# Kernel optimization log

Hardware: AMD Instinct MI355X
Metric: run time of the kernel (lower is better)

The kernel has to match this reference:

```python
import jax, jax.numpy as jnp
import numpy as np

B, GS, IN, HID = 256, 32, 512, 1024
HW = GS * GS

def setup_inputs() -> dict:
    key = jax.random.key(0)
    ks = jax.random.split(key, 18)
    s = 0.02
    return {
        "grid": jax.random.normal(ks[0], (B, 1, GS, GS), jnp.float32),
        "conv1_w": jax.random.normal(ks[1], (8, 1, 3, 3), jnp.float32) * s,
        "conv1_b": jax.random.normal(ks[2], (8,), jnp.float32) * s,
        "conv2_w": jax.random.normal(ks[3], (16, 8, 3, 3), jnp.float32) * s,
        "conv2_b": jax.random.normal(ks[4], (16,), jnp.float32) * s,
        "lin_w": jax.random.normal(ks[5], (IN, HW * 16), jnp.float32) * s,
        "lin_b": jax.random.normal(ks[6], (IN,), jnp.float32) * s,
        "gru_wih": jax.random.normal(ks[7], (3 * HID, IN + HW + 1), jnp.float32) * s,
        "gru_whh": jax.random.normal(ks[8], (3 * HID, HID), jnp.float32) * s,
        "gru_bih": jax.random.normal(ks[9], (3 * HID,), jnp.float32) * s,
        "gru_bhh": jax.random.normal(ks[10], (3 * HID,), jnp.float32) * s,
        "write_w": jax.random.normal(ks[11], (HW, HID), jnp.float32) * s,
        "write_b": jax.random.normal(ks[12], (HW,), jnp.float32) * s,
        "inc_w": jax.random.normal(ks[13], (1, HID), jnp.float32) * s,
        "inc_b": jax.random.normal(ks[14], (1,), jnp.float32) * s,
        "term_w": jax.random.normal(ks[15], (1, HID), jnp.float32) * s,
        "term_b": jax.random.normal(ks[16], (1,), jnp.float32) * s,
        "max_steps": 100,
    }

def _conv(x, w, b):
    y = jax.lax.conv_general_dilated(x, w, (1, 1), "SAME",
                                     dimension_numbers=("NCHW", "OIHW", "NCHW"))
    return y + b[None, :, None, None]

def _gru_cell(x, h, wih, whh, bih, bhh):
    gi = x @ wih.T + bih            # (B, 3H)
    gh = h @ whh.T + bhh
    ir, iz, inn = jnp.split(gi, 3, axis=1)
    hr, hz, hn = jnp.split(gh, 3, axis=1)
    r = jax.nn.sigmoid(ir + hr)
    z = jax.nn.sigmoid(iz + hz)
    n = jnp.tanh(inn + r * hn)
    return (1.0 - z) * n + z * h

def reference(grid, conv1_w, conv1_b, conv2_w, conv2_b, lin_w, lin_b,
              gru_wih, gru_whh, gru_bih, gru_bhh,
              write_w, write_b, inc_w, inc_b, term_w, term_b, max_steps):
    bsz = grid.shape[0]
    feat = jax.nn.relu(_conv(grid, conv1_w, conv1_b))
    feat = jax.nn.relu(_conv(feat, conv2_w, conv2_b))
    feat = feat.reshape(bsz, -1) @ lin_w.T + lin_b     # (B, IN), torch Flatten is channel-major

    def step(carry, _):
        h, mask, count, done = carry
        x = jnp.concatenate([feat, mask, count], axis=1)
        h2 = _gru_cell(x, h, gru_wih, gru_whh, gru_bih, gru_bhh)
        write = jax.nn.sigmoid(h2 @ write_w.T + write_b)
        inc = jax.nn.sigmoid(h2 @ inc_w.T + inc_b)
        term = jax.nn.sigmoid(h2 @ term_w.T + term_b)
        upd = jnp.logical_not(done)
        h_n = jnp.where(upd, h2, h)
        mask_n = jnp.where(upd, mask + write, mask)
        count_n = jnp.where(upd, count + inc, count)
        done_n = jnp.logical_or(done, jnp.all(term > 0.5))
        return (h_n, mask_n, count_n, done_n), None

    init = (jnp.zeros((bsz, HID), grid.dtype),
            jnp.zeros((bsz, HW), grid.dtype),
            jnp.zeros((bsz, 1), grid.dtype),
            jnp.array(False))
    (h, mask, count, done), _ = jax.lax.scan(step, init, None, length=max_steps)
    return count, mask
```

## Files before the change

kernel.cpp:

```cpp
#include <hip/hip_runtime.h>
#include <hip/hip_cooperative_groups.h>

namespace cg = cooperative_groups;

#define DEVI static __device__ __forceinline__

typedef __attribute__((ext_vector_type(8))) short s8v;
typedef __attribute__((ext_vector_type(4))) float f32x4;
typedef unsigned short us_t;
typedef unsigned int u32;

constexpr int NT_ = 256;
constexpr int B_ = 256, HW_ = 1024, IN_ = 512, HID_ = 1024, H3_ = 3072;
constexpr int XD_ = 1537;
constexpr int FLAT_ = 16384;

constexpr int OFF_WIHFBF = 0;
constexpr int OFF_WIHM2  = 393216;
constexpr int OFF_WHHBF  = 3538944;
constexpr int OFF_WIHC   = 5111808;
constexpr int OFF_CNTD   = 5114880;
constexpr int OFF_FLAGS  = 5115136;
constexpr int OFF_FEATBF = 5115264;
constexpr int OFF_GI     = 5180800;
constexpr int OFF_GH     = 5967232;
constexpr int OFF_H0     = 6753664;
constexpr int OFF_H1     = 7015808;
constexpr int OFF_WSIG   = 7277952;
constexpr int OFF_HHI    = 7540096;
constexpr int OFF_WSIG2  = 7671168;
constexpr int OFF_C2BF   = 7933312;
constexpr int OFF_LINWBF = 10030464;
constexpr int OFF_PART = OFF_GI;
constexpr int OFF_PA   = OFF_C2BF;
constexpr int OFF_WWBF = 10292608;

struct Params {
  const float* grid;
  const float* c1w; const float* c1b;
  const float* c2w; const float* c2b;
  const float* linw; const float* linb;
  const float* wih; const float* whh;
  const float* bih; const float* bhh;
  const float* ww;  const float* wb;
  const float* incw; const float* incb;
  const float* termw; const float* termb;
  const int* max_steps;
  float* out;
  float* ws;
};

DEVI float sigm(float x) { return 1.f / (1.f + __expf(-x)); }
DEVI float tanh_(float x) { return 1.f - 2.f / (__expf(2.f * x) + 1.f); }
DEVI float2 ld2(const float* p) { return *(const float2*)p; }
DEVI void ld4(float* d, const float* p) {
  float4 v = *(const float4*)p; d[0] = v.x; d[1] = v.y; d[2] = v.z; d[3] = v.w;
}
DEVI us_t f2bf(float x) {
  union { float f; u32 u; } v; v.f = x;
  u32 r = v.u + 0x7FFFu + ((v.u >> 16) & 1u);
  return (us_t)(r >> 16);
}
DEVI float bf2f(us_t h) {
  union { u32 u; float f; } v; v.u = ((u32)h) << 16; return v.f;
}
DEVI u32 pack2(float a, float b) { return (u32)f2bf(a) | ((u32)f2bf(b) << 16); }

__global__ __launch_bounds__(NT_) void conv_kernel(Params p) {
  __shared__ float s_in[34 * 34];
  __shared__ float s_c1[8 * 34 * 34];
  const int b = blockIdx.x;
  const int tid = threadIdx.x;
  for (int i = tid; i < 34 * 34; i += NT_) s_in[i] = 0.f;
  for (int i = tid; i < 8 * 34 * 34; i += NT_) s_c1[i] = 0.f;
  __syncthreads();
  for (int i = tid; i < 1024; i += NT_) {
    int y = i >> 5, x = i & 31;
    s_in[(y + 1) * 34 + (x + 1)] = p.grid[b * 1024 + i];
  }
  __syncthreads();
  const int pos0 = tid * 4;
  const int y = pos0 >> 5, x0 = pos0 & 31;
  {
    float win[3][6];
    #pragma unroll
    for (int dy = 0; dy < 3; ++dy)
      #pragma unroll
      for (int c = 0; c < 6; ++c) win[dy][c] = s_in[(y + dy) * 34 + x0 + c];
    float acc[8][4];
    #pragma unroll
    for (int oc = 0; oc < 8; ++oc)
      #pragma unroll
      for (int i = 0; i < 4; ++i) acc[oc][i] = p.c1b[oc];
    #pragma unroll
    for (int oc = 0; oc < 8; ++oc)
      #pragma unroll
      for (int dy = 0; dy < 3; ++dy)
        #pragma unroll
        for (int dx = 0; dx < 3; ++dx) {
          float w = p.c1w[oc * 9 + dy * 3 + dx];
          #pragma unroll
          for (int i = 0; i < 4; ++i)
            acc[oc][i] = fmaf(w, win[dy][i + dx], acc[oc][i]);
        }
    #pragma unroll
    for (int oc = 0; oc < 8; ++oc)
      #pragma unroll
      for (int i = 0; i < 4; ++i)
        s_c1[oc * 1156 + (y + 1) * 34 + (x0 + i + 1)] = fmaxf(acc[oc][i], 0.f);
  }
  __syncthreads();
  {
    float acc[16][4];
    #pragma unroll
    for (int oc = 0; oc < 16; ++oc)
      #pragma unroll
      for (int i = 0; i < 4; ++i) acc[oc][i] = p.c2b[oc];
    for (int ic = 0; ic < 8; ++ic) {
      float win[3][6];
      #pragma unroll
      for (int dy = 0; dy < 3; ++dy)
        #pragma unroll
        for (int c = 0; c < 6; ++c)
          win[dy][c] = s_c1[ic * 1156 + (y + dy) * 34 + x0 + c];
      #pragma unroll
      for (int oc = 0; oc < 16; ++oc)
        #pragma unroll
        for (int dy = 0; dy < 3; ++dy)
          #pragma unroll
          for (int dx = 0; dx < 3; ++dx) {
            float w = p.c2w[oc * 72 + ic * 9 + dy * 3 + dx];
            #pragma unroll
            for (int i = 0; i < 4; ++i)
              acc[oc][i] = fmaf(w, win[dy][i + dx], acc[oc][i]);
          }
    }
    us_t* dst = (us_t*)(p.ws + OFF_C2BF) + b * FLAT_;
    #pragma unroll
    for (int oc = 0; oc < 16; ++oc) {
      u32 lo = pack2(fmaxf(acc[oc][0], 0.f), fmaxf(acc[oc][1], 0.f));
      u32 hi = pack2(fmaxf(acc[oc][2], 0.f), fmaxf(acc[oc][3], 0.f));
      *(uint2*)(dst + oc * 1024 + pos0) = make_uint2(lo, hi);
    }
  }
}

__global__ __launch_bounds__(NT_) void prep_kernel(Params p) {
  const int gt = blockIdx.x * NT_ + threadIdx.x;
  const int gs = gridDim.x * NT_;
  us_t* wihf = (us_t*)(p.ws + OFF_WIHFBF);
  us_t* wihm2 = (us_t*)(p.ws + OFF_WIHM2);
  us_t* whhbf = (us_t*)(p.ws + OFF_WHHBF);
  us_t* linwbf = (us_t*)(p.ws + OFF_LINWBF);
  float* wihc = p.ws + OFF_WIHC;
  int* flags = (int*)(p.ws + OFF_FLAGS);
  for (int i = gt; i < (IN_ * FLAT_) / 4; i += gs) {
    float4 v = *(const float4*)(p.linw + (size_t)i * 4);
    *(uint2*)(linwbf + (size_t)i * 4) = make_uint2(pack2(v.x, v.y), pack2(v.z, v.w));
  }
  for (int i = gt; i < (H3_ * HID_) / 4; i += gs) {
    float4 v = *(const float4*)(p.whh + (size_t)i * 4);
    *(uint2*)(whhbf + (size_t)i * 4) = make_uint2(pack2(v.x, v.y), pack2(v.z, v.w));
  }
  for (int i = gt; i < H3_ * IN_; i += gs) {
    int n = i >> 9, k = i & 511;
    wihf[i] = f2bf(p.wih[n * XD_ + k]);
  }
  for (int i = gt; i < H3_ * HID_; i += gs) {
    int n = i >> 10, k = i & 1023;
    float v = p.wih[n * XD_ + 512 + k];
    us_t hi = f2bf(v);
    wihm2[n * 2048 + k] = hi;
    wihm2[n * 2048 + 1024 + k] = f2bf(v - bf2f(hi));
  }
  for (int i = gt; i < H3_; i += gs) wihc[i] = p.wih[i * XD_ + 1536];
  for (int i = gt; i < 128; i += gs) flags[i] = 1;
}

DEVI void mfma_block(const us_t* __restrict__ Ag, int lda,
                     const us_t* __restrict__ Bg, int ldb, int nc,
                     us_t* __restrict__ sA, us_t* __restrict__ sB,
                     float* __restrict__ dst, int ldd) {
  const int tid = threadIdx.x;
  const int ar = tid >> 3, au = tid & 7;
  const int sw = au ^ (ar & 7);
  const int abase = (ar * 8 + sw) * 8;
  const us_t* a0p = Ag + (size_t)ar * lda + au * 8;
  const us_t* a1p = Ag + (size_t)(ar + 32) * lda + au * 8;
  const us_t* b0p = Bg + (size_t)ar * ldb + au * 8;
  const us_t* b1p = b0p + (size_t)32 * ldb;
  const us_t* b2p = b0p + (size_t)64 * ldb;
  const us_t* b3p = b0p + (size_t)96 * ldb;
  f32x4 acc[4][2];
  #pragma unroll
  for (int f = 0; f < 4; ++f) { acc[f][0] = (f32x4)0.f; acc[f][1] = (f32x4)0.f; }
  s8v ra0 = *(const s8v*)a0p;
  s8v ra1 = *(const s8v*)a1p;
  s8v rb0 = *(const s8v*)b0p;
  s8v rb1 = *(const s8v*)b1p;
  s8v rb2 = *(const s8v*)b2p;
  s8v rb3 = *(const s8v*)b3p;
  const int w = tid >> 6;
  const int lane = tid & 63;
  const int l15 = lane & 15, l4 = lane >> 4;
  const int rsw = l15 & 7;
  int c = 0;
  for (;;) {
    __syncthreads();
    *(s8v*)(sA + abase) = ra0;
    *(s8v*)(sA + abase + 2048) = ra1;
    *(s8v*)(sB + abase) = rb0;
    *(s8v*)(sB + abase + 2048) = rb1;
    *(s8v*)(sB + abase + 4096) = rb2;
    *(s8v*)(sB + abase + 6144) = rb3;
    ++c;
    if (c < nc) {
      const int ko = c * 64;
      ra0 = *(const s8v*)(a0p + ko);
      ra1 = *(const s8v*)(a1p + ko);
      rb0 = *(const s8v*)(b0p + ko);
      rb1 = *(const s8v*)(b1p + ko);
      rb2 = *(const s8v*)(b2p + ko);
      rb3 = *(const s8v*)(b3p + ko);
    }
    __syncthreads();
    #pragma unroll
    for (int kk = 0; kk < 2; ++kk) {
      const int uoff = ((kk * 4 + l4) ^ rsw) * 8;
      s8v bA = *(const s8v*)(sB + (w * 32 + l15) * 64 + uoff);
      s8v bB = *(const s8v*)(sB + (w * 32 + 16 + l15) * 64 + uoff);
      #pragma unroll
      for (int f = 0; f < 4; ++f) {
        s8v a = *(const s8v*)(sA + (f * 16 + l15) * 64 + uoff);
        acc[f][0] = __builtin_amdgcn_mfma_f32_16x16x32_bf16(a, bA, acc[f][0], 0, 0, 0);
        acc[f][1] = __builtin_amdgcn_mfma_f32_16x16x32_bf16(a, bB, acc[f][1], 0, 0, 0);
      }
    }
    if (c >= nc) break;
  }
  #pragma unroll
  for (int f = 0; f < 4; ++f)
    #pragma unroll
    for (int g = 0; g < 2; ++g) {
      float* dp = dst + (size_t)(f * 16 + l4 * 4) * ldd + w * 32 + g * 16 + l15;
      #pragma unroll
      for (int j = 0; j < 4; ++j) dp[(size_t)j * ldd] = acc[f][g][j];
    }
}

__global__ __launch_bounds__(NT_) void lin_mfma(Params p) {
  __shared__ us_t sm[12288];
  const int b = blockIdx.x;
  const int ks = b & 15, t = b >> 4;
  const int mt = t >> 2, nt = t & 3;
  const us_t* A = (us_t*)(p.ws + OFF_C2BF) + (size_t)mt * 64 * FLAT_ + ks * 1024;
  const us_t* B = (us_t*)(p.ws + OFF_LINWBF) + (size_t)nt * 128 * FLAT_ + ks * 1024;
  float* dst = p.ws + OFF_PART + ks * (B_ * IN_) + mt * 64 * IN_ + nt * 128;
  mfma_block(A, FLAT_, B, FLAT_, 16, sm, sm + 4096, dst, IN_);
}

__global__ __launch_bounds__(NT_) void red_kernel(Params p) {
  const int gt = blockIdx.x * NT_ + threadIdx.x;
  {
    const int o = gt & (IN_ - 1);
    const float* part = p.ws + OFF_PART;
    float s = p.linb[o];
    #pragma unroll
    for (int ks = 0; ks < 16; ++ks) s += part[ks * (B_ * IN_) + gt];
    ((us_t*)(p.ws + OFF_FEATBF))[gt] = f2bf(s);
  }
  us_t* wwbf = (us_t*)(p.ws + OFF_WWBF);
  #pragma unroll
  for (int r = 0; r < 2; ++r) {
    const int j = gt + r * 131072;
    float4 v = *(const float4*)(p.ww + (size_t)j * 4);
    *(uint2*)(wwbf + (size_t)j * 4) = make_uint2(pack2(v.x, v.y), pack2(v.z, v.w));
  }
}

__global__ __launch_bounds__(NT_) void a1_mfma(Params p) {
  __shared__ us_t sm[12288];
  const int b = blockIdx.x;
  const int mt = b / 24, nt = b - mt * 24;
  const us_t* A = (us_t*)(p.ws + OFF_FEATBF) + (size_t)mt * 64 * IN_;
  const us_t* B = (us_t*)(p.ws + OFF_WIHFBF) + (size_t)nt * 128 * IN_;
  float* dst = p.ws + OFF_GI + (size_t)mt * 64 * H3_ + nt * 128;
  mfma_block(A, IN_, B, IN_, 8, sm, sm + 4096, dst, H3_);
}

__global__ __launch_bounds__(NT_) void stepA_mfma(Params p, int step) {
  if (((volatile int*)(p.ws + OFF_FLAGS))[step - 1]) return;
  __shared__ us_t sm[12288];
  const int b = blockIdx.x;
  if (b < 288) {
    const int term = b / 96, r = b - term * 96;
    const int mt = r / 24, nt = r - mt * 24;
    const us_t* A = (us_t*)(p.ws + OFF_WSIG2) + (size_t)mt * 64 * 2048 +
                    (term == 1 ? 1024 : 0);
    const us_t* B = (us_t*)(p.ws + OFF_WIHM2) + (size_t)nt * 128 * 2048 +
                    (term == 2 ? 1024 : 0);
    float* dst = p.ws + OFF_PA + (size_t)term * (B_ * H3_) + (size_t)mt * 64 * H3_ + nt * 128;
    mfma_block(A, 2048, B, 2048, 16, sm, sm + 4096, dst, H3_);
  } else {
    const int r = b - 288;
    const int mt = r / 24, nt = r - mt * 24;
    const us_t* A = (us_t*)(p.ws + OFF_HHI) + (size_t)mt * 64 * HID_;
    const us_t* B = (us_t*)(p.ws + OFF_WHHBF) + (size_t)nt * 128 * HID_;
    float* dst = p.ws + OFF_GH + (size_t)mt * 64 * H3_ + nt * 128;
    mfma_block(A, HID_, B, HID_, 16, sm, sm + 4096, dst, H3_);
  }
}

__global__ __launch_bounds__(NT_) void stepG_kernel(Params p, int step) {
  int* flags = (int*)(p.ws + OFF_FLAGS);
  if (step > 0 && ((volatile int*)flags)[step - 1]) return;
  __shared__ float sred[8];
  const int row = blockIdx.x;
  const int tid = threadIdx.x;
  const size_t base = (size_t)row * H3_;
  float* const gi = p.ws + OFF_GI + base;
  const float* const gh = p.ws + OFF_GH + base;
  const float* const pA = p.ws + OFF_PA;
  const float* const wihc = p.ws + OFF_WIHC;
  const float* hold = p.ws + ((step & 1) ? OFF_H1 : OFF_H0) + (size_t)row * HID_;
  float* hnew = p.ws + ((step & 1) ? OFF_H0 : OFF_H1) + (size_t)row * HID_;
  us_t* hhi = (us_t*)(p.ws + OFF_HHI) + (size_t)row * HID_;
  const float cd = (step > 0) ? (p.ws + OFF_CNTD)[row] : 0.f;
  float incd = 0.f, termd = 0.f;
  #pragma unroll
  for (int q = 0; q < 4; ++q) {
    const int c = tid + q * NT_;
    float gr_ = gi[c], gz_ = gi[1024 + c], gn_ = gi[2048 + c];
    float hr_ = 0.f, hz_ = 0.f, hn_ = 0.f, hv = 0.f;
    if (step > 0) {
      gr_ += pA[base + c] + pA[786432 + base + c] + pA[1572864 + base + c] +
             cd * wihc[c];
      gz_ += pA[base + 1024 + c] + pA[786432 + base + 1024 + c] +
             pA[1572864 + base + 1024 + c] + cd * wihc[1024 + c];
      gn_ += pA[base + 2048 + c] + pA[786432 + base + 2048 + c] +
             pA[1572864 + base + 2048 + c] + cd * wihc[2048 + c];
      gi[c] = gr_; gi[1024 + c] = gz_; gi[2048 + c] = gn_;
      hr_ = gh[c]; hz_ = gh[1024 + c]; hn_ = gh[2048 + c];
      hv = hold[c];
    }
    float rr = sigm(gr_ + p.bih[c] + hr_ + p.bhh[c]);
    float zz = sigm(gz_ + p.bih[1024 + c] + hz_ + p.bhh[1024 + c]);
    float nn = tanh_(gn_ + p.bih[2048 + c] + rr * (hn_ + p.bhh[2048 + c]));
    float h2 = (1.f - zz) * nn + zz * hv;
    hnew[c] = h2;
    hhi[c] = f2bf(h2);
    incd = fmaf(h2, p.incw[c], incd);
    termd = fmaf(h2, p.termw[c], termd);
  }
  #pragma unroll
  for (int off = 32; off > 0; off >>= 1) {
    incd += __shfl_down(incd, off);
    termd += __shfl_down(termd, off);
  }
  if ((tid & 63) == 0) { sred[tid >> 6] = incd; sred[4 + (tid >> 6)] = termd; }
  __syncthreads();
  if (tid == 0) {
    float it = sred[0] + sred[1] + sred[2] + sred[3];
    float tt = sred[4] + sred[5] + sred[6] + sred[7];
    float cdn = sigm(it + p.incb[0]);
    (p.ws + OFF_CNTD)[row] = cdn;
    p.out[row] += cdn;
    if (tt + p.termb[0] <= 0.f) atomicAnd(&flags[step], 0);
  }
}

__global__ __launch_bounds__(NT_) void stepW_mfma(Params p, int step) {
  if (step > 0 && ((volatile int*)(p.ws + OFF_FLAGS))[step - 1]) return;
  __shared__ us_t sm[12288];
  const int b = blockIdx.x;
  const int ks = b & 7, t = b >> 3;
  const int mt = t >> 3, nt = t & 7;
  const us_t* A = (us_t*)(p.ws + OFF_HHI) + (size_t)mt * 64 * HID_ + ks * 128;
  const us_t* B = (us_t*)(p.ws + OFF_WWBF) + (size_t)nt * 128 * HID_ + ks * 128;
  float* dst = p.ws + OFF_PA + ks * (B_ * HW_) + (size_t)mt * 64 * HW_ + nt * 128;
  mfma_block(A, HID_, B, HID_, 2, sm, sm + 4096, dst, HW_);
}

__global__ __launch_bounds__(NT_) void stepWepi_kernel(Params p, int step) {
  if (step > 0 && ((volatile int*)(p.ws + OFF_FLAGS))[step - 1]) return;
  const int i = (blockIdx.x * NT_ + threadIdx.x) * 4;
  const int m = i >> 10, n = i & 1023;
  const float* pW = p.ws + OFF_PA;
  float4 s = *(const float4*)(p.wb + n);
  #pragma unroll
  for (int ks = 0; ks < 8; ++ks) {
    float4 v = *(const float4*)(pW + ks * (B_ * HW_) + i);
    s.x += v.x; s.y += v.y; s.z += v.z; s.w += v.w;
  }
  float4 sv = {sigm(s.x), sigm(s.y), sigm(s.z), sigm(s.w)};
  float* op = p.out + B_ + i;
  float4 ov = *(float4*)op;
  ov.x += sv.x; ov.y += sv.y; ov.z += sv.z; ov.w += sv.w;
  *(float4*)op = ov;
  *(float4*)(p.ws + OFF_WSIG + i) = sv;
  us_t* w2 = (us_t*)(p.ws + OFF_WSIG2) + (size_t)m * 2048 + n;
  us_t h0 = f2bf(sv.x), h1 = f2bf(sv.y), h2b = f2bf(sv.z), h3 = f2bf(sv.w);
  *(uint2*)w2 = make_uint2((u32)h0 | ((u32)h1 << 16), (u32)h2b | ((u32)h3 << 16));
  *(uint2*)(w2 + 1024) = make_uint2(
      pack2(sv.x - bf2f(h0), sv.y - bf2f(h1)),
      pack2(sv.z - bf2f(h2b), sv.w - bf2f(h3)));
}

DEVI void b_job(const Params& p, float* sh2, float* swb,
                const float* gi, const float* gh, const float* hold,
                float* hnew, float* wsig, float* cntd, int* dflag, int job) {
  const int tid = threadIdx.x;
  const int mt = job >> 3, nt = job & 7;
  const int r0 = mt * 8, c0 = nt * 128;
  const int gr = tid >> 5;
  const int gk = (tid & 31) * 2;
  const int wr = tid & 7;
  const int wc = (tid >> 3) * 4;
  const int row = r0 + gr;
  const float* giR = gi + row * H3_;
  const float* ghR = gh + row * H3_;
  const float* hR = hold + row * HID_;
  float* hW = hnew + row * HID_;
  float acc[4] = {0.f, 0.f, 0.f, 0.f};
  float incd = 0.f, termd = 0.f;
  const bool wh = (nt == 0);
  for (int kc = 0; kc < HID_; kc += 64) {
    float2 gxr = ld2(giR + kc + gk);
    float2 gxz = ld2(giR + 1024 + kc + gk);
    float2 gxn = ld2(giR + 2048 + kc + gk);
    float2 ghr = ld2(ghR + kc + gk);
    float2 ghz = ld2(ghR + 1024 + kc + gk);
    float2 ghn = ld2(ghR + 2048 + kc + gk);
    float2 hol = ld2(hR + kc + gk);
    float2 bri = ld2(p.bih + kc + gk);
    float2 brh = ld2(p.bhh + kc + gk);
    float2 bzi = ld2(p.bih + 1024 + kc + gk);
    float2 bzh = ld2(p.bhh + 1024 + kc + gk);
    float2 bni = ld2(p.bih + 2048 + kc + gk);
    float2 bnh = ld2(p.bhh + 2048 + kc + gk);
    float2 iw = ld2(p.incw + kc + gk);
    float2 tw = ld2(p.termw + kc + gk);
    float h2[2];
    {
      float rr = sigm(gxr.x + bri.x + ghr.x + brh.x);
      float zz = sigm(gxz.x + bzi.x + ghz.x + bzh.x);
      float nn = tanh_(gxn.x + bni.x + rr * (ghn.x + bnh.x));
      h2[0] = (1.f - zz) * nn + zz * hol.x;
      rr = sigm(gxr.y + bri.y + ghr.y + brh.y);
      zz = sigm(gxz.y + bzi.y + ghz.y + bzh.y);
      nn = tanh_(gxn.y + bni.y + rr * (ghn.y + bnh.y));
      h2[1] = (1.f - zz) * nn + zz * hol.y;
    }
    incd = fmaf(h2[0], iw.x, fmaf(h2[1], iw.y, incd));
    termd = fmaf(h2[0], tw.x, fmaf(h2[1], tw.y, termd));
    float4 wreg[8];
    #pragma unroll
    for (int it = 0; it < 8; ++it) {
      int id = tid + it * 256;
      int c = id >> 4, k4 = (id & 15) * 4;
      wreg[it] = *(const float4*)(p.ww + (c0 + c) * HID_ + kc + k4);
    }
    __syncthreads();
    sh2[gr * 68 + gk] = h2[0];
    sh2[gr * 68 + gk + 1] = h2[1];
    #pragma unroll
    for (int it = 0; it < 8; ++it) {
      int id = tid + it * 256;
      int c = id >> 4, k4 = (id & 15) * 4;
      swb[(k4 + 0) * 132 + c] = wreg[it].x;
      swb[(k4 + 1) * 132 + c] = wreg[it].y;
      swb[(k4 + 2) * 132 + c] = wreg[it].z;
      swb[(k4 + 3) * 132 + c] = wreg[it].w;
    }
    if (wh) {
      *(float2*)(hW + kc + gk) = make_float2(h2[0], h2[1]);
      *(u32*)((us_t*)(p.ws + OFF_HHI) + row * HID_ + kc + gk) = pack2(h2[0], h2[1]);
    }
    __syncthreads();
    #pragma unroll 8
    for (int kk = 0; kk < 64; ++kk) {
      float a = sh2[wr * 68 + kk];
      float4 b = *(const float4*)(swb + kk * 132 + wc);
      acc[0] = fmaf(a, b.x, acc[0]);
      acc[1] = fmaf(a, b.y, acc[1]);
      acc[2] = fmaf(a, b.z, acc[2]);
      acc[3] = fmaf(a, b.w, acc[3]);
    }
  }
  if (wh) {
    #pragma unroll
    for (int off = 16; off > 0; off >>= 1) {
      incd += __shfl_down(incd, off, 32);
      termd += __shfl_down(termd, off, 32);
    }
    if ((tid & 31) == 0) {
      float cd = sigm(incd + p.incb[0]);
      cntd[row] = cd;
      p.out[row] += cd;
      if (termd + p.termb[0] <= 0.f) atomicAnd(dflag, 0);
    }
  }
  {
    const int m = r0 + wr;
    float4 wb4 = *(const float4*)(p.wb + c0 + wc);
    float4 sv = {sigm(acc[0] + wb4.x), sigm(acc[1] + wb4.y),
                 sigm(acc[2] + wb4.z), sigm(acc[3] + wb4.w)};
    float* op = p.out + B_ + m * HW_ + c0 + wc;
    float4 ov = *(float4*)op;
    ov.x += sv.x; ov.y += sv.y; ov.z += sv.z; ov.w += sv.w;
    *(float4*)op = ov;
    *(float4*)(wsig + m * HID_ + c0 + wc) = sv;
    us_t* w2 = (us_t*)(p.ws + OFF_WSIG2) + m * 2048 + c0 + wc;
    us_t h0 = f2bf(sv.x), h1 = f2bf(sv.y), h2b = f2bf(sv.z), h3 = f2bf(sv.w);
    *(uint2*)w2 = make_uint2((u32)h0 | ((u32)h1 << 16), (u32)h2b | ((u32)h3 << 16));
    *(uint2*)(w2 + 1024) = make_uint2(
        pack2(sv.x - bf2f(h0), sv.y - bf2f(h1)),
        pack2(sv.z - bf2f(h2b), sv.w - bf2f(h3)));
  }
}

template <bool SB>
DEVI void gemm_db64(const float* __restrict__ A, int lda,
                    const float* __restrict__ Bw, int ldb, int K,
                    float* __restrict__ As, float* __restrict__ Bs,
                    float (&acc)[4][4]) {
  constexpr int P = 68;
  const int tid = threadIdx.x;
  const int tx = tid & 15, ty = tid >> 4;
  const int lr = tid >> 2, lk = (tid & 3) << 2;
  #pragma unroll
  for (int i = 0; i < 4; ++i)
    #pragma unroll
    for (int j = 0; j < 4; ++j) acc[i][j] = 0.f;
  auto ldb4 = [&](int k0) {
    float4 v;
    if constexpr (SB) {
      const float* q = Bw + (size_t)lr * ldb + k0 + lk;
      v.x = q[0]; v.y = q[1]; v.z = q[2]; v.w = q[3];
    } else {
      v = *(const float4*)(Bw + (size_t)lr * ldb + k0 + lk);
    }
    return v;
  };
  float4 va = *(const float4*)(A + lr * lda + lk);
  float4 vb = ldb4(0);
  As[(lk + 0) * P + lr] = va.x; As[(lk + 1) * P + lr] = va.y;
  As[(lk + 2) * P + lr] = va.z; As[(lk + 3) * P + lr] = va.w;
  Bs[(lk + 0) * P + lr] = vb.x; Bs[(lk + 1) * P + lr] = vb.y;
  Bs[(lk + 2) * P + lr] = vb.z; Bs[(lk + 3) * P + lr] = vb.w;
  __syncthreads();
  int cur = 0;
  for (int k0 = 16; k0 < K; k0 += 16) {
    va = *(const float4*)(A + lr * lda + k0 + lk);
    vb = ldb4(k0);
    const float* as = As + cur * (16 * P);
    const float* bs = Bs + cur * (16 * P);
    #pragma unroll
    for (int kk = 0; kk < 16; ++kk) {
      float a[4], b[4];
      ld4(a, as + kk * P + ty * 4);
      ld4(b, bs + kk * P + tx * 4);
      #pragma unroll
      for (int i = 0; i < 4; ++i)
        #pragma unroll
        for (int j = 0; j < 4; ++j) acc[i][j] = fmaf(a[i], b[j], acc[i][j]);
    }
    __syncthreads();
    float* asw = As + (cur ^ 1) * (16 * P);
    float* bsw = Bs + (cur ^ 1) * (16 * P);
    asw[(lk + 0) * P + lr] = va.x; asw[(lk + 1) * P + lr] = va.y;
    asw[(lk + 2) * P + lr] = va.z; asw[(lk + 3) * P + lr] = va.w;
    bsw[(lk + 0) * P + lr] = vb.x; bsw[(lk + 1) * P + lr] = vb.y;
    bsw[(lk + 2) * P + lr] = vb.z; bsw[(lk + 3) * P + lr] = vb.w;
    __syncthreads();
    cur ^= 1;
  }
  const float* as = As + cur * (16 * P);
  const float* bs = Bs + cur * (16 * P);
  #pragma unroll
  for (int kk = 0; kk < 16; ++kk) {
    float a[4], b[4];
    ld4(a, as + kk * P + ty * 4);
    ld4(b, bs + kk * P + tx * 4);
    #pragma unroll
    for (int i = 0; i < 4; ++i)
      #pragma unroll
      for (int j = 0; j < 4; ++j) acc[i][j] = fmaf(a[i], b[j], acc[i][j]);
  }
}

__global__ __launch_bounds__(NT_, 2) void tail_kernel(Params p, int start) {
  int* flags = (int*)(p.ws + OFF_FLAGS);
  if (((volatile int*)flags)[start - 1]) return;
  cg::grid_group gg = cg::this_grid();
  __shared__ __align__(16) float smem[8992];
  float* As = smem;
  float* Bs = smem + 2176;
  float* sh2 = smem;
  float* swb = smem + 544;
  float* const ws = p.ws;
  float* const gi = ws + OFF_GI;
  float* const gh = ws + OFF_GH;
  float* const wsig = ws + OFF_WSIG;
  float* const cntd = ws + OFF_CNTD;
  const float* const wihc = ws + OFF_WIHC;
  const int tid = threadIdx.x;
  const int bid = blockIdx.x;
  const int nb = gridDim.x;
  const int tx = tid & 15, ty = tid >> 4;
  const int msteps = p.max_steps[0];

  for (int step = start; step < msteps; ++step) {
    float* hcur = ws + ((step & 1) ? OFF_H1 : OFF_H0);
    float* hnxt = ws + ((step & 1) ? OFF_H0 : OFF_H1);
    for (int job = bid; job < 384; job += nb) {
      float acc[4][4];
      if (job < 192) {
        const int mt = job / 48, nt = job - mt * 48;
        gemm_db64<true>(wsig + mt * 64 * HID_, HID_,
                        p.wih + (size_t)nt * 64 * XD_ + 512, XD_, HID_, As, Bs, acc);
        #pragma unroll
        for (int i = 0; i < 4; ++i) {
          const int m = mt * 64 + ty * 4 + i;
          const float cd = cntd[m];
          float4 wc4 = *(const float4*)(wihc + nt * 64 + tx * 4);
          float* gp = gi + m * H3_ + nt * 64 + tx * 4;
          float4 g = *(float4*)gp;
          g.x += acc[i][0] + cd * wc4.x;
          g.y += acc[i][1] + cd * wc4.y;
          g.z += acc[i][2] + cd * wc4.z;
          g.w += acc[i][3] + cd * wc4.w;
          *(float4*)gp = g;
        }
      } else {
        const int j = job - 192;
        const int mt = j / 48, nt = j - mt * 48;
        gemm_db64<false>(hcur + mt * 64 * HID_, HID_,
                         p.whh + (size_t)nt * 64 * HID_, HID_, HID_, As, Bs, acc);
        #pragma unroll
        for (int i = 0; i < 4; ++i) {
          float4 v = {acc[i][0], acc[i][1], acc[i][2], acc[i][3]};
          *(float4*)(gh + (mt * 64 + ty * 4 + i) * H3_ + nt * 64 + tx * 4) = v;
        }
      }
      __syncthreads();
    }
    gg.sync();
    for (int job = bid; job < 256; job += nb)
      b_job(p, sh2, swb, gi, gh, hcur, hnxt, wsig, cntd, &flags[step], job);
    gg.sync();
    if (((volatile int*)flags)[step]) break;
  }
}

extern "C" void kernel_launch(void* const* d_in, const int* in_sizes, int n_in,
                              void* d_out, int out_size, void* d_ws, size_t ws_size,
                              hipStream_t stream) {
  (void)in_sizes; (void)n_in; (void)ws_size;
  Params prm;
  prm.grid = (const float*)d_in[0];
  prm.c1w  = (const float*)d_in[1];
  prm.c1b  = (const float*)d_in[2];
  prm.c2w  = (const float*)d_in[3];
  prm.c2b  = (const float*)d_in[4];
  prm.linw = (const float*)d_in[5];
  prm.linb = (const float*)d_in[6];
  prm.wih  = (const float*)d_in[7];
  prm.whh  = (const float*)d_in[8];
  prm.bih  = (const float*)d_in[9];
  prm.bhh  = (const float*)d_in[10];
  prm.ww   = (const float*)d_in[11];
  prm.wb   = (const float*)d_in[12];
  prm.incw = (const float*)d_in[13];
  prm.incb = (const float*)d_in[14];
  prm.termw = (const float*)d_in[15];
  prm.termb = (const float*)d_in[16];
  prm.max_steps = (const int*)d_in[17];
  prm.out = (float*)d_out;
  prm.ws = (float*)d_ws;

  hipLaunchKernelGGL(conv_kernel, dim3(B_), dim3(NT_), 0, stream, prm);
  hipLaunchKernelGGL(prep_kernel, dim3(2048), dim3(NT_), 0, stream, prm);
  hipLaunchKernelGGL(lin_mfma, dim3(256), dim3(NT_), 0, stream, prm);
  hipLaunchKernelGGL(red_kernel, dim3(512), dim3(NT_), 0, stream, prm);
  hipMemsetAsync(d_out, 0, (size_t)out_size * sizeof(float), stream);
  hipLaunchKernelGGL(a1_mfma, dim3(96), dim3(NT_), 0, stream, prm);

  constexpr int U = 3;
  hipLaunchKernelGGL(stepG_kernel, dim3(B_), dim3(NT_), 0, stream, prm, 0);
  hipLaunchKernelGGL(stepW_mfma, dim3(256), dim3(NT_), 0, stream, prm, 0);
  hipLaunchKernelGGL(stepWepi_kernel, dim3(256), dim3(NT_), 0, stream, prm, 0);
  for (int t = 1; t < U; ++t) {
    hipLaunchKernelGGL(stepA_mfma, dim3(384), dim3(NT_), 0, stream, prm, t);
    hipLaunchKernelGGL(stepG_kernel, dim3(B_), dim3(NT_), 0, stream, prm, t);
    hipLaunchKernelGGL(stepW_mfma, dim3(256), dim3(NT_), 0, stream, prm, t);
    hipLaunchKernelGGL(stepWepi_kernel, dim3(256), dim3(NT_), 0, stream, prm, t);
  }
  int start = U;
  void* args[] = {(void*)&prm, (void*)&start};
  (void)hipLaunchCooperativeKernel((const void*)tail_kernel, dim3(384), dim3(NT_),
                                   args, 0, stream);
}
```

Before: 155.5 us.

## Fuse conv and prep kernels, split-K stepA GEMMs, drop output memset

Merges the conv and weight-prep kernels into one launch with block-index dispatch, and splits the stepA GEMMs along K into two halves (768 blocks instead of 384), writing eight partial buffers that stepG sums. The output memset is removed; step 0 now writes the outputs directly instead of accumulating. The number of unrolled multi-kernel steps before the cooperative tail kernel drops from 3 to 2. Together these aim to cut launch overhead and raise GPU occupancy for the per-step GEMMs, at the cost of extra partial-sum traffic and a larger workspace.

```diff
diff --git a/kernel.cpp b/kernel.cpp
--- a/kernel.cpp
+++ b/kernel.cpp
@@ -32,8 +32,9 @@
 constexpr int OFF_C2BF   = 7933312;
 constexpr int OFF_LINWBF = 10030464;
 constexpr int OFF_PART = OFF_GI;
-constexpr int OFF_PA   = OFF_C2BF;
+constexpr int OFF_PW   = OFF_C2BF;
 constexpr int OFF_WWBF = 10292608;
+constexpr int OFF_PA2  = 14224768;
 
 struct Params {
   const float* grid;
@@ -66,115 +67,116 @@
 }
 DEVI u32 pack2(float a, float b) { return (u32)f2bf(a) | ((u32)f2bf(b) << 16); }
 
-__global__ __launch_bounds__(NT_) void conv_kernel(Params p) {
-  __shared__ float s_in[34 * 34];
-  __shared__ float s_c1[8 * 34 * 34];
-  const int b = blockIdx.x;
+__global__ __launch_bounds__(NT_) void front_kernel(Params p) {
+  __shared__ float smem[34 * 34 + 8 * 34 * 34];
   const int tid = threadIdx.x;
-  for (int i = tid; i < 34 * 34; i += NT_) s_in[i] = 0.f;
-  for (int i = tid; i < 8 * 34 * 34; i += NT_) s_c1[i] = 0.f;
-  __syncthreads();
-  for (int i = tid; i < 1024; i += NT_) {
-    int y = i >> 5, x = i & 31;
-    s_in[(y + 1) * 34 + (x + 1)] = p.grid[b * 1024 + i];
-  }
-  __syncthreads();
-  const int pos0 = tid * 4;
-  const int y = pos0 >> 5, x0 = pos0 & 31;
-  {
-    float win[3][6];
-    #pragma unroll
-    for (int dy = 0; dy < 3; ++dy)
-      #pragma unroll
-      for (int c = 0; c < 6; ++c) win[dy][c] = s_in[(y + dy) * 34 + x0 + c];
-    float acc[8][4];
-    #pragma unroll
-    for (int oc = 0; oc < 8; ++oc)
-      #pragma unroll
-      for (int i = 0; i < 4; ++i) acc[oc][i] = p.c1b[oc];
-    #pragma unroll
-    for (int oc = 0; oc < 8; ++oc)
+  if (blockIdx.x < 256) {
+    float* s_in = smem;
+    float* s_c1 = smem + 34 * 34;
+    const int b = blockIdx.x;
+    for (int i = tid; i < 34 * 34; i += NT_) s_in[i] = 0.f;
+    for (int i = tid; i < 8 * 34 * 34; i += NT_) s_c1[i] = 0.f;
+    __syncthreads();
+    for (int i = tid; i < 1024; i += NT_) {
+      int y = i >> 5, x = i & 31;
+      s_in[(y + 1) * 34 + (x + 1)] = p.grid[b * 1024 + i];
+    }
+    __syncthreads();
+    const int pos0 = tid * 4;
+    const int y = pos0 >> 5, x0 = pos0 & 31;
+    {
+      float win[3][6];
       #pragma unroll
       for (int dy = 0; dy < 3; ++dy)
         #pragma unroll
-        for (int dx = 0; dx < 3; ++dx) {
-          float w = p.c1w[oc * 9 + dy * 3 + dx];
-          #pragma unroll
-          for (int i = 0; i < 4; ++i)
-            acc[oc][i] = fmaf(w, win[dy][i + dx], acc[oc][i]);
-        }
-    #pragma unroll
-    for (int oc = 0; oc < 8; ++oc)
-      #pragma unroll
-      for (int i = 0; i < 4; ++i)
-        s_c1[oc * 1156 + (y + 1) * 34 + (x0 + i + 1)] = fmaxf(acc[oc][i], 0.f);
-  }
-  __syncthreads();
-  {
-    float acc[16][4];
-    #pragma unroll
-    for (int oc = 0; oc < 16; ++oc)
-      #pragma unroll
-      for (int i = 0; i < 4; ++i) acc[oc][i] = p.c2b[oc];
-    for (int ic = 0; ic < 8; ++ic) {
-      float win[3][6];
-      #pragma unroll
-      for (int dy = 0; dy < 3; ++dy)
-        #pragma unroll
-        for (int c = 0; c < 6; ++c)
-          win[dy][c] = s_c1[ic * 1156 + (y + dy) * 34 + x0 + c];
-      #pragma unroll
-      for (int oc = 0; oc < 16; ++oc)
+        for (int c = 0; c < 6; ++c) win[dy][c] = s_in[(y + dy) * 34 + x0 + c];
+      float acc[8][4];
+      #pragma unroll
+      for (int oc = 0; oc < 8; ++oc)
+        #pragma unroll
+        for (int i = 0; i < 4; ++i) acc[oc][i] = p.c1b[oc];
+      #pragma unroll
+      for (int oc = 0; oc < 8; ++oc)
         #pragma unroll
         for (int dy = 0; dy < 3; ++dy)
           #pragma unroll
           for (int dx = 0; dx < 3; ++dx) {
-            float w = p.c2w[oc * 72 + ic * 9 + dy * 3 + dx];
+            float w = p.c1w[oc * 9 + dy * 3 + dx];
             #pragma unroll
             for (int i = 0; i < 4; ++i)
               acc[oc][i] = fmaf(w, win[dy][i + dx], acc[oc][i]);
           }
-    }
-    us_t* dst = (us_t*)(p.ws + OFF_C2BF) + b * FLAT_;
-    #pragma unroll
-    for (int oc = 0; oc < 16; ++oc) {
-      u32 lo = pack2(fmaxf(acc[oc][0], 0.f), fmaxf(acc[oc][1], 0.f));
-      u32 hi = pack2(fmaxf(acc[oc][2], 0.f), fmaxf(acc[oc][3], 0.f));
-      *(uint2*)(dst + oc * 1024 + pos0) = make_uint2(lo, hi);
-    }
-  }
-}
-
-__global__ __launch_bounds__(NT_) void prep_kernel(Params p) {
-  const int gt = blockIdx.x * NT_ + threadIdx.x;
-  const int gs = gridDim.x * NT_;
-  us_t* wihf = (us_t*)(p.ws + OFF_WIHFBF);
-  us_t* wihm2 = (us_t*)(p.ws + OFF_WIHM2);
-  us_t* whhbf = (us_t*)(p.ws + OFF_WHHBF);
-  us_t* linwbf = (us_t*)(p.ws + OFF_LINWBF);
-  float* wihc = p.ws + OFF_WIHC;
-  int* flags = (int*)(p.ws + OFF_FLAGS);
-  for (int i = gt; i < (IN_ * FLAT_) / 4; i += gs) {
-    float4 v = *(const float4*)(p.linw + (size_t)i * 4);
-    *(uint2*)(linwbf + (size_t)i * 4) = make_uint2(pack2(v.x, v.y), pack2(v.z, v.w));
-  }
-  for (int i = gt; i < (H3_ * HID_) / 4; i += gs) {
-    float4 v = *(const float4*)(p.whh + (size_t)i * 4);
-    *(uint2*)(whhbf + (size_t)i * 4) = make_uint2(pack2(v.x, v.y), pack2(v.z, v.w));
-  }
-  for (int i = gt; i < H3_ * IN_; i += gs) {
-    int n = i >> 9, k = i & 511;
-    wihf[i] = f2bf(p.wih[n * XD_ + k]);
-  }
-  for (int i = gt; i < H3_ * HID_; i += gs) {
-    int n = i >> 10, k = i & 1023;
-    float v = p.wih[n * XD_ + 512 + k];
-    us_t hi = f2bf(v);
-    wihm2[n * 2048 + k] = hi;
-    wihm2[n * 2048 + 1024 + k] = f2bf(v - bf2f(hi));
-  }
-  for (int i = gt; i < H3_; i += gs) wihc[i] = p.wih[i * XD_ + 1536];
-  for (int i = gt; i < 128; i += gs) flags[i] = 1;
+      #pragma unroll
+      for (int oc = 0; oc < 8; ++oc)
+        #pragma unroll
+        for (int i = 0; i < 4; ++i)
+          s_c1[oc * 1156 + (y + 1) * 34 + (x0 + i + 1)] = fmaxf(acc[oc][i], 0.f);
+    }
+    __syncthreads();
+    {
+      float acc[16][4];
+      #pragma unroll
+      for (int oc = 0; oc < 16; ++oc)
+        #pragma unroll
+        for (int i = 0; i < 4; ++i) acc[oc][i] = p.c2b[oc];
+      for (int ic = 0; ic < 8; ++ic) {
+        float win[3][6];
+        #pragma unroll
+        for (int dy = 0; dy < 3; ++dy)
+          #pragma unroll
+          for (int c = 0; c < 6; ++c)
+            win[dy][c] = s_c1[ic * 1156 + (y + dy) * 34 + x0 + c];
+        #pragma unroll
+        for (int oc = 0; oc < 16; ++oc)
+          #pragma unroll
+          for (int dy = 0; dy < 3; ++dy)
+            #pragma unroll
+            for (int dx = 0; dx < 3; ++dx) {
+              float w = p.c2w[oc * 72 + ic * 9 + dy * 3 + dx];
+              #pragma unroll
+              for (int i = 0; i < 4; ++i)
+                acc[oc][i] = fmaf(w, win[dy][i + dx], acc[oc][i]);
+            }
+      }
+      us_t* dst = (us_t*)(p.ws + OFF_C2BF) + b * FLAT_;
+      #pragma unroll
+      for (int oc = 0; oc < 16; ++oc) {
+        u32 lo = pack2(fmaxf(acc[oc][0], 0.f), fmaxf(acc[oc][1], 0.f));
+        u32 hi = pack2(fmaxf(acc[oc][2], 0.f), fmaxf(acc[oc][3], 0.f));
+        *(uint2*)(dst + oc * 1024 + pos0) = make_uint2(lo, hi);
+      }
+    }
+  } else {
+    const int gt = (blockIdx.x - 256) * NT_ + tid;
+    const int gs = 2048 * NT_;
+    us_t* wihf = (us_t*)(p.ws + OFF_WIHFBF);
+    us_t* wihm2 = (us_t*)(p.ws + OFF_WIHM2);
+    us_t* whhbf = (us_t*)(p.ws + OFF_WHHBF);
+    us_t* linwbf = (us_t*)(p.ws + OFF_LINWBF);
+    float* wihc = p.ws + OFF_WIHC;
+    int* flags = (int*)(p.ws + OFF_FLAGS);
+    for (int i = gt; i < (IN_ * FLAT_) / 4; i += gs) {
+      float4 v = *(const float4*)(p.linw + (size_t)i * 4);
+      *(uint2*)(linwbf + (size_t)i * 4) = make_uint2(pack2(v.x, v.y), pack2(v.z, v.w));
+    }
+    for (int i = gt; i < (H3_ * HID_) / 4; i += gs) {
+      float4 v = *(const float4*)(p.whh + (size_t)i * 4);
+      *(uint2*)(whhbf + (size_t)i * 4) = make_uint2(pack2(v.x, v.y), pack2(v.z, v.w));
+    }
+    for (int i = gt; i < H3_ * IN_; i += gs) {
+      int n = i >> 9, k = i & 511;
+      wihf[i] = f2bf(p.wih[n * XD_ + k]);
+    }
+    for (int i = gt; i < H3_ * HID_; i += gs) {
+      int n = i >> 10, k = i & 1023;
+      float v = p.wih[n * XD_ + 512 + k];
+      us_t hi = f2bf(v);
+      wihm2[n * 2048 + k] = hi;
+      wihm2[n * 2048 + 1024 + k] = f2bf(v - bf2f(hi));
+    }
+    for (int i = gt; i < H3_; i += gs) wihc[i] = p.wih[i * XD_ + 1536];
+    for (int i = gt; i < 128; i += gs) flags[i] = 1;
+  }
 }
 
 DEVI void mfma_block(const us_t* __restrict__ Ag, int lda,
@@ -292,22 +294,29 @@
   if (((volatile int*)(p.ws + OFF_FLAGS))[step - 1]) return;
   __shared__ us_t sm[12288];
   const int b = blockIdx.x;
-  if (b < 288) {
-    const int term = b / 96, r = b - term * 96;
-    const int mt = r / 24, nt = r - mt * 24;
+  if (b < 576) {
+    const int term = b / 192;
+    const int r = b - term * 192;
+    const int ks = r / 96;
+    const int t = r - ks * 96;
+    const int mt = t / 24, nt = t - mt * 24;
     const us_t* A = (us_t*)(p.ws + OFF_WSIG2) + (size_t)mt * 64 * 2048 +
-                    (term == 1 ? 1024 : 0);
+                    (term == 1 ? 1024 : 0) + ks * 512;
     const us_t* B = (us_t*)(p.ws + OFF_WIHM2) + (size_t)nt * 128 * 2048 +
-                    (term == 2 ? 1024 : 0);
-    float* dst = p.ws + OFF_PA + (size_t)term * (B_ * H3_) + (size_t)mt * 64 * H3_ + nt * 128;
-    mfma_block(A, 2048, B, 2048, 16, sm, sm + 4096, dst, H3_);
+                    (term == 2 ? 1024 : 0) + ks * 512;
+    float* dst = p.ws + OFF_PA2 + (size_t)(term * 2 + ks) * 786432 +
+                 (size_t)mt * 64 * H3_ + nt * 128;
+    mfma_block(A, 2048, B, 2048, 8, sm, sm + 4096, dst, H3_);
   } else {
-    const int r = b - 288;
-    const int mt = r / 24, nt = r - mt * 24;
-    const us_t* A = (us_t*)(p.ws + OFF_HHI) + (size_t)mt * 64 * HID_;
-    const us_t* B = (us_t*)(p.ws + OFF_WHHBF) + (size_t)nt * 128 * HID_;
-    float* dst = p.ws + OFF_GH + (size_t)mt * 64 * H3_ + nt * 128;
-    mfma_block(A, HID_, B, HID_, 16, sm, sm + 4096, dst, H3_);
+    const int r = b - 576;
+    const int ks = r / 96;
+    const int t = r - ks * 96;
+    const int mt = t / 24, nt = t - mt * 24;
+    const us_t* A = (us_t*)(p.ws + OFF_HHI) + (size_t)mt * 64 * HID_ + ks * 512;
+    const us_t* B = (us_t*)(p.ws + OFF_WHHBF) + (size_t)nt * 128 * HID_ + ks * 512;
+    float* dst = p.ws + OFF_PA2 + (size_t)(6 + ks) * 786432 +
+                 (size_t)mt * 64 * H3_ + nt * 128;
+    mfma_block(A, HID_, B, HID_, 8, sm, sm + 4096, dst, H3_);
   }
 }
 
@@ -319,8 +328,7 @@
   const int tid = threadIdx.x;
   const size_t base = (size_t)row * H3_;
   float* const gi = p.ws + OFF_GI + base;
-  const float* const gh = p.ws + OFF_GH + base;
-  const float* const pA = p.ws + OFF_PA;
+  const float* const pA = p.ws + OFF_PA2;
   const float* const wihc = p.ws + OFF_WIHC;
   const float* hold = p.ws + ((step & 1) ? OFF_H1 : OFF_H0) + (size_t)row * HID_;
   float* hnew = p.ws + ((step & 1) ? OFF_H0 : OFF_H1) + (size_t)row * HID_;
@@ -333,14 +341,20 @@
     float gr_ = gi[c], gz_ = gi[1024 + c], gn_ = gi[2048 + c];
     float hr_ = 0.f, hz_ = 0.f, hn_ = 0.f, hv = 0.f;
     if (step > 0) {
-      gr_ += pA[base + c] + pA[786432 + base + c] + pA[1572864 + base + c] +
-             cd * wihc[c];
-      gz_ += pA[base + 1024 + c] + pA[786432 + base + 1024 + c] +
-             pA[1572864 + base + 1024 + c] + cd * wihc[1024 + c];
-      gn_ += pA[base + 2048 + c] + pA[786432 + base + 2048 + c] +
-             pA[1572864 + base + 2048 + c] + cd * wihc[2048 + c];
+      #pragma unroll
+      for (int t6 = 0; t6 < 6; ++t6) {
+        const float* pp = pA + (size_t)t6 * 786432 + base;
+        gr_ += pp[c]; gz_ += pp[1024 + c]; gn_ += pp[2048 + c];
+      }
+      gr_ += cd * wihc[c];
+      gz_ += cd * wihc[1024 + c];
+      gn_ += cd * wihc[2048 + c];
+      const float* q6 = pA + (size_t)6 * 786432 + base;
+      const float* q7 = pA + (size_t)7 * 786432 + base;
+      hr_ = q6[c] + q7[c];
+      hz_ = q6[1024 + c] + q7[1024 + c];
+      hn_ = q6[2048 + c] + q7[2048 + c];
       gi[c] = gr_; gi[1024 + c] = gz_; gi[2048 + c] = gn_;
-      hr_ = gh[c]; hz_ = gh[1024 + c]; hn_ = gh[2048 + c];
       hv = hold[c];
     }
     float rr = sigm(gr_ + p.bih[c] + hr_ + p.bhh[c]);
@@ -364,7 +378,8 @@
     float tt = sred[4] + sred[5] + sred[6] + sred[7];
     float cdn = sigm(it + p.incb[0]);
     (p.ws + OFF_CNTD)[row] = cdn;
-    p.out[row] += cdn;
+    if (step == 0) p.out[row] = cdn;
+    else p.out[row] += cdn;
     if (tt + p.termb[0] <= 0.f) atomicAnd(&flags[step], 0);
   }
 }
@@ -377,7 +392,7 @@
   const int mt = t >> 3, nt = t & 7;
   const us_t* A = (us_t*)(p.ws + OFF_HHI) + (size_t)mt * 64 * HID_ + ks * 128;
   const us_t* B = (us_t*)(p.ws + OFF_WWBF) + (size_t)nt * 128 * HID_ + ks * 128;
-  float* dst = p.ws + OFF_PA + ks * (B_ * HW_) + (size_t)mt * 64 * HW_ + nt * 128;
+  float* dst = p.ws + OFF_PW + ks * (B_ * HW_) + (size_t)mt * 64 * HW_ + nt * 128;
   mfma_block(A, HID_, B, HID_, 2, sm, sm + 4096, dst, HW_);
 }
 
@@ -385,7 +400,7 @@
   if (step > 0 && ((volatile int*)(p.ws + OFF_FLAGS))[step - 1]) return;
   const int i = (blockIdx.x * NT_ + threadIdx.x) * 4;
   const int m = i >> 10, n = i & 1023;
-  const float* pW = p.ws + OFF_PA;
+  const float* pW = p.ws + OFF_PW;
   float4 s = *(const float4*)(p.wb + n);
   #pragma unroll
   for (int ks = 0; ks < 8; ++ks) {
@@ -394,9 +409,13 @@
   }
   float4 sv = {sigm(s.x), sigm(s.y), sigm(s.z), sigm(s.w)};
   float* op = p.out + B_ + i;
-  float4 ov = *(float4*)op;
-  ov.x += sv.x; ov.y += sv.y; ov.z += sv.z; ov.w += sv.w;
-  *(float4*)op = ov;
+  if (step == 0) {
+    *(float4*)op = sv;
+  } else {
+    float4 ov = *(float4*)op;
+    ov.x += sv.x; ov.y += sv.y; ov.z += sv.z; ov.w += sv.w;
+    *(float4*)op = ov;
+  }
   *(float4*)(p.ws + OFF_WSIG + i) = sv;
   us_t* w2 = (us_t*)(p.ws + OFF_WSIG2) + (size_t)m * 2048 + n;
   us_t h0 = f2bf(sv.x), h1 = f2bf(sv.y), h2b = f2bf(sv.z), h3 = f2bf(sv.w);
@@ -656,7 +675,7 @@
 extern "C" void kernel_launch(void* const* d_in, const int* in_sizes, int n_in,
                               void* d_out, int out_size, void* d_ws, size_t ws_size,
                               hipStream_t stream) {
-  (void)in_sizes; (void)n_in; (void)ws_size;
+  (void)in_sizes; (void)n_in; (void)out_size; (void)ws_size;
   Params prm;
   prm.grid = (const float*)d_in[0];
   prm.c1w  = (const float*)d_in[1];
@@ -679,19 +698,17 @@
   prm.out = (float*)d_out;
   prm.ws = (float*)d_ws;
 
-  hipLaunchKernelGGL(conv_kernel, dim3(B_), dim3(NT_), 0, stream, prm);
-  hipLaunchKernelGGL(prep_kernel, dim3(2048), dim3(NT_), 0, stream, prm);
+  hipLaunchKernelGGL(front_kernel, dim3(2304), dim3(NT_), 0, stream, prm);
   hipLaunchKernelGGL(lin_mfma, dim3(256), dim3(NT_), 0, stream, prm);
   hipLaunchKernelGGL(red_kernel, dim3(512), dim3(NT_), 0, stream, prm);
-  hipMemsetAsync(d_out, 0, (size_t)out_size * sizeof(float), stream);
   hipLaunchKernelGGL(a1_mfma, dim3(96), dim3(NT_), 0, stream, prm);
 
-  constexpr int U = 3;
+  constexpr int U = 2;
   hipLaunchKernelGGL(stepG_kernel, dim3(B_), dim3(NT_), 0, stream, prm, 0);
   hipLaunchKernelGGL(stepW_mfma, dim3(256), dim3(NT_), 0, stream, prm, 0);
   hipLaunchKernelGGL(stepWepi_kernel, dim3(256), dim3(NT_), 0, stream, prm, 0);
   for (int t = 1; t < U; ++t) {
-    hipLaunchKernelGGL(stepA_mfma, dim3(384), dim3(NT_), 0, stream, prm, t);
+    hipLaunchKernelGGL(stepA_mfma, dim3(768), dim3(NT_), 0, stream, prm, t);
     hipLaunchKernelGGL(stepG_kernel, dim3(B_), dim3(NT_), 0, stream, prm, t);
     hipLaunchKernelGGL(stepW_mfma, dim3(256), dim3(NT_), 0, stream, prm, t);
     hipLaunchKernelGGL(stepWepi_kernel, dim3(256), dim3(NT_), 0, stream, prm, t);
```

New measurement: 138.8 us (median of 2 runs). 10.7% less time.
